# Kernel tuning notes

Measured on AMD Instinct MI355X. Metric: run time of the kernel, lower is better.

Reference implementation:

```python
import jax, jax.numpy as jnp
import numpy as np

DIM = 1024
SEQ_LEN = 2048
NUM_HEAD = 16
HEAD_DIM = 64
B = 4


def setup_inputs() -> dict:
    key = jax.random.key(0)
    ks = jax.random.split(key, 9)
    hd = NUM_HEAD * HEAD_DIM
    s_in = 1.0 / np.sqrt(DIM)
    s_o = 1.0 / np.sqrt(hd)
    return {
        "x": jax.random.normal(ks[0], (B, SEQ_LEN, DIM), dtype=jnp.float32),
        "q_w": jax.random.uniform(ks[1], (hd, DIM), jnp.float32, -s_in, s_in),
        "q_b": jax.random.uniform(ks[2], (hd,), jnp.float32, -s_in, s_in),
        "k_w": jax.random.uniform(ks[3], (hd, DIM), jnp.float32, -s_in, s_in),
        "k_b": jax.random.uniform(ks[4], (hd,), jnp.float32, -s_in, s_in),
        "v_w": jax.random.uniform(ks[5], (hd, DIM), jnp.float32, -s_in, s_in),
        "v_b": jax.random.uniform(ks[6], (hd,), jnp.float32, -s_in, s_in),
        "o_w": jax.random.uniform(ks[7], (DIM, hd), jnp.float32, -s_o, s_o),
        "o_b": jax.random.uniform(ks[8], (DIM,), jnp.float32, -s_o, s_o),
    }


def reference(x, q_w, q_b, k_w, k_b, v_w, v_b, o_w, o_b):
    Bn, T, C = x.shape
    # QKV projections (torch Linear: x @ W^T + b)
    q = (x @ q_w.T + q_b).reshape(Bn, T, NUM_HEAD, HEAD_DIM).transpose(0, 2, 1, 3)
    k = (x @ k_w.T + k_b).reshape(Bn, T, NUM_HEAD, HEAD_DIM).transpose(0, 2, 1, 3)
    v = (x @ v_w.T + v_b).reshape(Bn, T, NUM_HEAD, HEAD_DIM).transpose(0, 2, 1, 3)
    scale = HEAD_DIM ** -0.5
    attn = jnp.einsum("bhqd,bhkd->bhqk", q, k) * scale  # (B,H,T,T)
    causal = jnp.tril(jnp.ones((T, T), dtype=bool))
    attn = jnp.where(causal[None, None, :, :], attn, -jnp.inf)
    p = jax.nn.softmax(attn, axis=-1)  # stable softmax (max-subtracted)
    out = jnp.einsum("bhqk,bhkd->bhqd", p, v)
    out = out.transpose(0, 2, 1, 3).reshape(Bn, T, NUM_HEAD * HEAD_DIM)
    return out @ o_w.T + o_b
```

## Files before the change

### kernel.cpp

```cpp
#include <hip/hip_runtime.h>
#include <stdint.h>

typedef short short8 __attribute__((ext_vector_type(8)));
typedef float f32x4 __attribute__((ext_vector_type(4)));
typedef float f32x16 __attribute__((ext_vector_type(16)));
typedef unsigned int uint2v __attribute__((ext_vector_type(2)));
typedef unsigned int uint4v __attribute__((ext_vector_type(4)));

__device__ __forceinline__ unsigned short f2bf(float f) {
    unsigned int u = __float_as_uint(f);
    u += 0x7fffu + ((u >> 16) & 1u);
    return (unsigned short)(u >> 16);
}

__device__ __forceinline__ void gld_lds16(const unsigned short* g, unsigned short* l) {
    __builtin_amdgcn_global_load_lds((const __attribute__((address_space(1))) unsigned int*)g,
                                     (__attribute__((address_space(3))) unsigned int*)l,
                                     16, 0, 0);
}

#define QSCL 0.18033688011112042f

__global__ __launch_bounds__(256) void cvt_all(const float* __restrict__ x,
                                               const float* __restrict__ qw, const float* __restrict__ kw,
                                               const float* __restrict__ vw, const float* __restrict__ ow,
                                               const float* __restrict__ qb, const float* __restrict__ kb,
                                               const float* __restrict__ vb,
                                               unsigned short* __restrict__ Xb,
                                               unsigned short* __restrict__ Wqkv,
                                               unsigned short* __restrict__ Owb,
                                               float* __restrict__ bqkv) {
    int i = blockIdx.x * 256 + threadIdx.x;
    const float* src; uint2* dst; int j;
    if (i < 2097152)      { src = x;  dst = (uint2*)Xb;                j = i; }
    else if (i < 2359296) { src = qw; dst = (uint2*)Wqkv;              j = i - 2097152; }
    else if (i < 2621440) { src = kw; dst = (uint2*)(Wqkv + 1048576);  j = i - 2359296; }
    else if (i < 2883584) { src = vw; dst = (uint2*)(Wqkv + 2097152);  j = i - 2621440; }
    else if (i < 3145728) { src = ow; dst = (uint2*)Owb;               j = i - 2883584; }
    else {
        int t = i - 3145728;
        const float4* bs = (t < 256) ? (const float4*)qb : (t < 512) ? (const float4*)kb : (const float4*)vb;
        ((float4*)bqkv)[t] = bs[t & 255];
        return;
    }
    float4 v = ((const float4*)src)[j];
    unsigned int lo = (unsigned int)f2bf(v.x) | ((unsigned int)f2bf(v.y) << 16);
    unsigned int hi = (unsigned int)f2bf(v.z) | ((unsigned int)f2bf(v.w) << 16);
    dst[j] = make_uint2(lo, hi);
}

template<int MODE>
__global__ __launch_bounds__(256) void gemm_bt(const unsigned short* __restrict__ A,
                                               const unsigned short* __restrict__ Bm,
                                               const float* __restrict__ bias,
                                               void* __restrict__ C0,
                                               unsigned short* __restrict__ VtOut,
                                               int M, int N, int K)
{
    __shared__ __align__(16) unsigned short As[128 * 64];
    __shared__ __align__(16) unsigned short Bs[128 * 64];
    const int tid  = threadIdx.x;
    const int bm   = blockIdx.x, bn = blockIdx.y;
    const int lane = tid & 63, w = tid >> 6;
    const int wm   = w >> 1, wn = w & 1;
    const int quad = lane >> 4, l15 = lane & 15;

    f32x4 acc[4][4];
#pragma unroll
    for (int mt = 0; mt < 4; mt++)
#pragma unroll
        for (int nt = 0; nt < 4; nt++)
            acc[mt][nt] = (f32x4){0.f, 0.f, 0.f, 0.f};

    const int kTiles = K >> 6;
    for (int kt = 0; kt < kTiles; ++kt) {
        __syncthreads();
#pragma unroll
        for (int i = 0; i < 4; i++) {
            int G  = i * 256 + tid;
            int m  = G >> 3, g = G & 7;
            int gs = g ^ (m & 7);
            int Gb = i * 256 + (w << 6);
            gld_lds16(A  + (size_t)(bm * 128 + m) * K + kt * 64 + gs * 8, &As[Gb * 8]);
            gld_lds16(Bm + (size_t)(bn * 128 + m) * K + kt * 64 + gs * 8, &Bs[Gb * 8]);
        }
        __syncthreads();
#pragma unroll
        for (int ks = 0; ks < 2; ++ks) {
            short8 af[4], bfr[4];
#pragma unroll
            for (int mt = 0; mt < 4; mt++) {
                int m = wm * 64 + mt * 16 + l15;
                af[mt] = *(const short8*)&As[m * 64 + (((ks * 4 + quad) ^ (l15 & 7)) << 3)];
            }
#pragma unroll
            for (int nt = 0; nt < 4; nt++) {
                int n = wn * 64 + nt * 16 + l15;
                bfr[nt] = *(const short8*)&Bs[n * 64 + (((ks * 4 + quad) ^ (l15 & 7)) << 3)];
            }
#pragma unroll
            for (int mt = 0; mt < 4; mt++)
#pragma unroll
                for (int nt = 0; nt < 4; nt++)
                    acc[mt][nt] = __builtin_amdgcn_mfma_f32_16x16x32_bf16(af[mt], bfr[nt], acc[mt][nt], 0, 0, 0);
        }
    }
    const int row0 = bm * 128 + wm * 64, col0 = bn * 128 + wn * 64;
#pragma unroll
    for (int nt = 0; nt < 4; nt++) {
        int col = col0 + nt * 16 + l15;
        float bv = bias[col];
#pragma unroll
        for (int mt = 0; mt < 4; mt++) {
            if (MODE == 1 && col >= 2048) {
                int row = row0 + mt * 16 + quad * 4;
                int b = row >> 11, t = row & 2047;
                ushort4 pk;
                pk.x = f2bf(acc[mt][nt][0] + bv);
                pk.y = f2bf(acc[mt][nt][1] + bv);
                pk.z = f2bf(acc[mt][nt][2] + bv);
                pk.w = f2bf(acc[mt][nt][3] + bv);
                *(ushort4*)(VtOut + (size_t)(b * 1024 + (col - 2048)) * 2048 + t) = pk;
            } else {
#pragma unroll
                for (int r = 0; r < 4; r++) {
                    int row = row0 + mt * 16 + quad * 4 + r;
                    float v = acc[mt][nt][r] + bv;
                    if (MODE == 1) {
                        if (col < 1024) v *= QSCL;
                        ((unsigned short*)C0)[(size_t)row * 2048 + col] = f2bf(v);
                    } else {
                        ((float*)C0)[(size_t)row * N + col] = v;
                    }
                }
            }
        }
    }
}

#define NEG_RAW (-1e30f)
__global__ __launch_bounds__(256, 4) void attn_mfma(const unsigned short* __restrict__ QK,
                                                    const unsigned short* __restrict__ Vt,
                                                    unsigned short* __restrict__ O)
{
    __shared__ __align__(16) unsigned short Kb[3][64 * 64];
    __shared__ __align__(16) unsigned short Vb[3][64 * 64];
    const int tid  = threadIdx.x;
    const int lane = tid & 63, w = tid >> 6;
    const int hi   = lane >> 5, l31 = lane & 31;
    const int s7   = lane & 7;
    const int bh   = blockIdx.x;
    const int b    = bh >> 4, h = bh & 15;
    const int qt   = (int)gridDim.y - 1 - (int)blockIdx.y;
    const int qbase = qt * 128 + w * 32;

    const unsigned short* Qp = QK + (size_t)(b * 2048) * 2048 + h * 64;
    const unsigned short* Kp = Qp + 1024;
    const unsigned short* Vp = Vt + (size_t)(bh * 64) * 2048;

    short8 qf[4];
    {
        const unsigned short* qrow = Qp + (size_t)(qbase + l31) * 2048 + hi * 8;
#pragma unroll
        for (int dk = 0; dk < 4; dk++)
            qf[dk] = *(const short8*)(qrow + dk * 16);
    }

    f32x16 oacc[2];
#pragma unroll
    for (int i = 0; i < 2; i++)
#pragma unroll
        for (int r = 0; r < 16; r++) oacc[i][r] = 0.f;
    float lsum = 0.f;

    const int ktend   = 2 * qt + 1;
    const int ktmax_w = (qbase + 31) >> 6;

    auto stage = [&](int t, int bi) {
#pragma unroll
        for (int i = 0; i < 2; i++) {
            int G = i * 256 + tid;
            int r = G >> 3, g = G & 7, gs = g ^ (r & 7);
            int Gb = i * 256 + (w << 6);
            gld_lds16(Kp + (size_t)(t * 64 + r) * 2048 + gs * 8, &Kb[bi][Gb * 8]);
            gld_lds16(Vp + (size_t)r * 2048 + t * 64 + gs * 8, &Vb[bi][Gb * 8]);
        }
    };

    stage(0, 0);
    stage(1, 1);

    int cur = 0;
    for (int kt = 0; kt <= ktend; ++kt) {
        if (kt < ktend) asm volatile("s_waitcnt vmcnt(4)" ::: "memory");
        else            asm volatile("s_waitcnt vmcnt(0)" ::: "memory");
        __builtin_amdgcn_sched_barrier(0);
        __builtin_amdgcn_s_barrier();
        __builtin_amdgcn_sched_barrier(0);
        if (kt + 2 <= ktend) {
            int bi = cur + 2; if (bi >= 3) bi -= 3;
            stage(kt + 2, bi);
        }
        if (kt <= ktmax_w) {
            __builtin_amdgcn_s_setprio(1);
            const unsigned short* Kc = Kb[cur];
            const unsigned short* Vc = Vb[cur];
            const int kbase = kt * 64;
#pragma unroll
            for (int sub = 0; sub < 2; sub++) {
                const int kb0 = kbase + sub * 32;
                if (kb0 > qbase + 31) continue;
                f32x16 sacc;
#pragma unroll
                for (int r = 0; r < 16; r++) sacc[r] = 0.f;
                const unsigned short* kr = &Kc[(sub * 32 + l31) * 64];
#pragma unroll
                for (int dk = 0; dk < 4; dk++) {
                    short8 kf = *(const short8*)(kr + (((dk * 2 + hi) ^ s7) << 3));
                    sacc = __builtin_amdgcn_mfma_f32_32x32x16_bf16(kf, qf[dk], sacc, 0, 0, 0);
                }
                if (kb0 + 31 > qbase) {
                    const int qg = qbase + l31;
                    const int kb = kb0 + 4 * hi;
#pragma unroll
                    for (int r = 0; r < 16; r++) {
                        int key = kb + (r & 3) + 8 * (r >> 2);
                        if (key > qg) sacc[r] = NEG_RAW;
                    }
                }
#pragma unroll
                for (int r = 0; r < 16; r++) sacc[r] = __builtin_exp2f(sacc[r]);
                {
                    float s0 = (sacc[0] + sacc[1]) + (sacc[2] + sacc[3]);
                    float s1 = (sacc[4] + sacc[5]) + (sacc[6] + sacc[7]);
                    float s2 = (sacc[8] + sacc[9]) + (sacc[10] + sacc[11]);
                    float s3 = (sacc[12] + sacc[13]) + (sacc[14] + sacc[15]);
                    lsum += (s0 + s1) + (s2 + s3);
                }
                unsigned int pk[8];
#pragma unroll
                for (int t2 = 0; t2 < 8; t2++)
                    pk[t2] = __builtin_amdgcn_perm(__float_as_uint(sacc[2 * t2 + 1]),
                                                   __float_as_uint(sacc[2 * t2]), 0x07060302u);
                uint2v r0 = __builtin_amdgcn_permlane32_swap(pk[0], pk[2], false, false);
                uint2v r1 = __builtin_amdgcn_permlane32_swap(pk[1], pk[3], false, false);
                uint2v r2 = __builtin_amdgcn_permlane32_swap(pk[4], pk[6], false, false);
                uint2v r3 = __builtin_amdgcn_permlane32_swap(pk[5], pk[7], false, false);
                short8 pf[2];
                { uint4v u; u.x = r0.x; u.y = r1.x; u.z = r0.y; u.w = r1.y; pf[0] = __builtin_bit_cast(short8, u); }
                { uint4v u; u.x = r2.x; u.y = r3.x; u.z = r2.y; u.w = r3.y; pf[1] = __builtin_bit_cast(short8, u); }
#pragma unroll
                for (int kv = 0; kv < 2; kv++) {
#pragma unroll
                    for (int dsub = 0; dsub < 2; dsub++) {
                        const int d = dsub * 32 + l31;
                        short8 vf = *(const short8*)&Vc[d * 64 + (((sub * 4 + kv * 2 + hi) ^ s7) << 3)];
                        oacc[dsub] = __builtin_amdgcn_mfma_f32_32x32x16_bf16(vf, pf[kv], oacc[dsub], 0, 0, 0);
                    }
                }
            }
            __builtin_amdgcn_s_setprio(0);
        }
        cur = (cur == 2) ? 0 : cur + 1;
    }

    uint2v lt = __builtin_amdgcn_permlane32_swap(__float_as_uint(lsum), __float_as_uint(lsum), false, false);
    const float inv = 1.f / (__uint_as_float(lt.x) + __uint_as_float(lt.y));
    unsigned short* op = O + (size_t)(b * 2048 + qbase + l31) * 1024 + h * 64;
#pragma unroll
    for (int dsub = 0; dsub < 2; dsub++) {
#pragma unroll
        for (int q4 = 0; q4 < 4; q4++) {
            ushort4 pkv;
            pkv.x = f2bf(oacc[dsub][q4 * 4 + 0] * inv);
            pkv.y = f2bf(oacc[dsub][q4 * 4 + 1] * inv);
            pkv.z = f2bf(oacc[dsub][q4 * 4 + 2] * inv);
            pkv.w = f2bf(oacc[dsub][q4 * 4 + 3] * inv);
            *(ushort4*)(op + dsub * 32 + q4 * 8 + hi * 4) = pkv;
        }
    }
}

extern "C" void kernel_launch(void* const* d_in, const int* in_sizes, int n_in,
                              void* d_out, int out_size, void* d_ws, size_t ws_size,
                              hipStream_t stream)
{
    const float* x   = (const float*)d_in[0];
    const float* q_w = (const float*)d_in[1];
    const float* q_b = (const float*)d_in[2];
    const float* k_w = (const float*)d_in[3];
    const float* k_b = (const float*)d_in[4];
    const float* v_w = (const float*)d_in[5];
    const float* v_b = (const float*)d_in[6];
    const float* o_w = (const float*)d_in[7];
    const float* o_b = (const float*)d_in[8];
    float* out = (float*)d_out;

    unsigned short* Xb   = (unsigned short*)d_ws;
    unsigned short* Wqkv = Xb + 8388608;
    unsigned short* Owb  = Wqkv + 3145728;
    float*          bqkv = (float*)(Owb + 1048576);
    unsigned short* QK   = (unsigned short*)(bqkv + 3072);
    unsigned short* Vtg  = QK + 16777216;
    unsigned short* Abf  = Vtg + 8388608;

    cvt_all<<<12291, 256, 0, stream>>>(x, q_w, k_w, v_w, o_w, q_b, k_b, v_b,
                                       Xb, Wqkv, Owb, bqkv);
    gemm_bt<1><<<dim3(64, 24), 256, 0, stream>>>(Xb, Wqkv, bqkv, QK, Vtg, 8192, 3072, 1024);
    attn_mfma<<<dim3(64, 16), 256, 0, stream>>>(QK, Vtg, Abf);
    gemm_bt<0><<<dim3(64, 8), 256, 0, stream>>>(Abf, Owb, o_b, out, nullptr, 8192, 1024, 1024);
}
```

Before: 255.2 us.

## Replace QKV projection GEMM with 256x256-tile, 8-wave pipelined kernel

After: 265.4 us. 1.04x slower.

```diff
diff --git a/kernel.cpp b/kernel.cpp
--- a/kernel.cpp
+++ b/kernel.cpp
@@ -138,6 +138,154 @@
     }
 }
 
+#define PIN() __builtin_amdgcn_sched_barrier(0)
+
+#define RD_A(BI, MH) \
+    _Pragma("unroll") for (int mtl = 0; mtl < 4; ++mtl) { \
+        int m = wm * 128 + (MH) * 64 + mtl * 16 + l15; \
+        af[mtl][0] = *(const short8*)&As[BI][m * 64 + ((quad ^ (m & 7)) << 3)]; \
+        af[mtl][1] = *(const short8*)&As[BI][m * 64 + (((4 + quad) ^ (m & 7)) << 3)]; \
+    }
+
+#define RD_B(BI, NH) \
+    _Pragma("unroll") for (int ntl = 0; ntl < 2; ++ntl) { \
+        int n = wn * 64 + ((NH) * 2 + ntl) * 16 + l15; \
+        bfv[(NH) * 2 + ntl][0] = *(const short8*)&Bs[BI][n * 64 + ((quad ^ (n & 7)) << 3)]; \
+        bfv[(NH) * 2 + ntl][1] = *(const short8*)&Bs[BI][n * 64 + (((4 + quad) ^ (n & 7)) << 3)]; \
+    }
+
+#define MFMA_Q(MH, NH) \
+    __builtin_amdgcn_s_barrier(); \
+    asm volatile("s_waitcnt lgkmcnt(0)" ::: "memory"); \
+    PIN(); \
+    __builtin_amdgcn_s_setprio(1); \
+    _Pragma("unroll") for (int mtl = 0; mtl < 4; ++mtl) \
+    _Pragma("unroll") for (int ntl = 0; ntl < 2; ++ntl) { \
+        const int nt_ = (NH) * 2 + ntl, mt_ = (MH) * 4 + mtl; \
+        acc[mt_][nt_] = __builtin_amdgcn_mfma_f32_16x16x32_bf16(af[mtl][0], bfv[nt_][0], acc[mt_][nt_], 0, 0, 0); \
+        acc[mt_][nt_] = __builtin_amdgcn_mfma_f32_16x16x32_bf16(af[mtl][1], bfv[nt_][1], acc[mt_][nt_], 0, 0, 0); \
+    } \
+    __builtin_amdgcn_s_setprio(0);
+
+#define ENDP() do { __builtin_amdgcn_s_barrier(); PIN(); } while (0)
+
+#define STAGE(DST, BI, H, SRC, KT) \
+    _Pragma("unroll") for (int i_ = 0; i_ < 2; ++i_) { \
+        int G_ = i_ * 512 + tid; \
+        int r_ = G_ >> 3, g_ = G_ & 7, gs_ = g_ ^ (r_ & 7); \
+        gld_lds16((SRC) + (size_t)((H) * 128 + r_) * K + (KT) * 64 + gs_ * 8, \
+                  &DST[BI][(H) * 8192 + (i_ * 512 + w * 64) * 8]); \
+    }
+
+template<int MODE>
+__global__ __launch_bounds__(512, 2) void gemm256(const unsigned short* __restrict__ A,
+                                                  const unsigned short* __restrict__ Bm,
+                                                  const float* __restrict__ bias,
+                                                  void* __restrict__ C0,
+                                                  unsigned short* __restrict__ VtOut,
+                                                  int M, int N, int K)
+{
+    __shared__ __align__(16) unsigned short As[2][256 * 64];
+    __shared__ __align__(16) unsigned short Bs[2][256 * 64];
+    const int tid  = threadIdx.x;
+    const int bm   = blockIdx.x, bn = blockIdx.y;
+    const int lane = tid & 63, w = tid >> 6;
+    const int wm   = w >> 2, wn = w & 3;
+    const int quad = lane >> 4, l15 = lane & 15;
+
+    const unsigned short* Ag = A  + (size_t)(bm * 256) * K;
+    const unsigned short* Bg = Bm + (size_t)(bn * 256) * K;
+
+    f32x4 acc[8][4];
+#pragma unroll
+    for (int mt = 0; mt < 8; mt++)
+#pragma unroll
+        for (int nt = 0; nt < 4; nt++)
+            acc[mt][nt] = (f32x4){0.f, 0.f, 0.f, 0.f};
+
+    short8 af[4][2];
+    short8 bfv[4][2];
+
+    const int NI = K >> 7;
+
+    STAGE(As, 0, 0, Ag, 0); STAGE(As, 0, 1, Ag, 0);
+    STAGE(Bs, 0, 0, Bg, 0); STAGE(Bs, 0, 1, Bg, 0);
+    STAGE(Bs, 1, 0, Bg, 1); STAGE(Bs, 1, 1, Bg, 1);
+    STAGE(As, 1, 0, Ag, 1); STAGE(As, 1, 1, Ag, 1);
+    asm volatile("s_waitcnt vmcnt(8)" ::: "memory");
+    __builtin_amdgcn_s_barrier();
+    PIN();
+
+    for (int j = 0; j < NI; ++j) {
+        const int t2 = 2 * j + 2, t3 = 2 * j + 3;
+        const bool more = (j < NI - 1);
+        RD_A(0, 0); RD_B(0, 0);
+        MFMA_Q(0, 0);
+        ENDP();
+        RD_B(0, 1);
+        MFMA_Q(0, 1);
+        ENDP();
+        RD_A(0, 1);
+        if (more) { STAGE(Bs, 0, 0, Bg, t2); }
+        MFMA_Q(1, 0);
+        ENDP();
+        if (more) { STAGE(Bs, 0, 1, Bg, t2); }
+        MFMA_Q(1, 1);
+        if (more) { asm volatile("s_waitcnt vmcnt(4)" ::: "memory"); }
+        else      { asm volatile("s_waitcnt vmcnt(0)" ::: "memory"); }
+        ENDP();
+        RD_A(1, 0); RD_B(1, 0);
+        if (more) { STAGE(As, 0, 0, Ag, t2); }
+        MFMA_Q(0, 0);
+        ENDP();
+        RD_B(1, 1);
+        if (more) { STAGE(As, 0, 1, Ag, t2); }
+        MFMA_Q(0, 1);
+        ENDP();
+        RD_A(1, 1);
+        if (more) { STAGE(Bs, 1, 0, Bg, t3); STAGE(Bs, 1, 1, Bg, t3); }
+        MFMA_Q(1, 0);
+        ENDP();
+        if (more) { STAGE(As, 1, 0, Ag, t3); STAGE(As, 1, 1, Ag, t3); }
+        MFMA_Q(1, 1);
+        if (more) { asm volatile("s_waitcnt vmcnt(8)" ::: "memory"); }
+        else      { asm volatile("s_waitcnt vmcnt(0)" ::: "memory"); }
+        ENDP();
+    }
+
+    const int row0 = bm * 256 + wm * 128, col0 = bn * 256 + wn * 64;
+#pragma unroll
+    for (int nt = 0; nt < 4; nt++) {
+        int col = col0 + nt * 16 + l15;
+        float bv = bias[col];
+#pragma unroll
+        for (int mt = 0; mt < 8; mt++) {
+            if (MODE == 1 && col >= 2048) {
+                int row = row0 + mt * 16 + quad * 4;
+                int b = row >> 11, t = row & 2047;
+                ushort4 pk;
+                pk.x = f2bf(acc[mt][nt][0] + bv);
+                pk.y = f2bf(acc[mt][nt][1] + bv);
+                pk.z = f2bf(acc[mt][nt][2] + bv);
+                pk.w = f2bf(acc[mt][nt][3] + bv);
+                *(ushort4*)(VtOut + (size_t)(b * 1024 + (col - 2048)) * 2048 + t) = pk;
+            } else {
+#pragma unroll
+                for (int r = 0; r < 4; r++) {
+                    int row = row0 + mt * 16 + quad * 4 + r;
+                    float v = acc[mt][nt][r] + bv;
+                    if (MODE == 1) {
+                        if (col < 1024) v *= QSCL;
+                        ((unsigned short*)C0)[(size_t)row * 2048 + col] = f2bf(v);
+                    } else {
+                        ((float*)C0)[(size_t)row * N + col] = v;
+                    }
+                }
+            }
+        }
+    }
+}
+
 #define NEG_RAW (-1e30f)
 __global__ __launch_bounds__(256, 4) void attn_mfma(const unsigned short* __restrict__ QK,
                                                     const unsigned short* __restrict__ Vt,
@@ -306,7 +454,7 @@
 
     cvt_all<<<12291, 256, 0, stream>>>(x, q_w, k_w, v_w, o_w, q_b, k_b, v_b,
                                        Xb, Wqkv, Owb, bqkv);
-    gemm_bt<1><<<dim3(64, 24), 256, 0, stream>>>(Xb, Wqkv, bqkv, QK, Vtg, 8192, 3072, 1024);
+    gemm256<1><<<dim3(32, 12), 512, 0, stream>>>(Xb, Wqkv, bqkv, QK, Vtg, 8192, 3072, 1024);
     attn_mfma<<<dim3(64, 16), 256, 0, stream>>>(QK, Vtg, Abf);
     gemm_bt<0><<<dim3(64, 8), 256, 0, stream>>>(Abf, Owb, o_b, out, nullptr, 8192, 1024, 1024);
 }
```

## Double attention query tile per wave and pair causal tiles for load balance

Applied to the files above, without the earlier changes.

Result: slower. 272.8 us (+6.9%).

```diff
diff --git a/kernel.cpp b/kernel.cpp
--- a/kernel.cpp
+++ b/kernel.cpp
@@ -139,7 +139,7 @@
 }
 
 #define NEG_RAW (-1e30f)
-__global__ __launch_bounds__(256, 4) void attn_mfma(const unsigned short* __restrict__ QK,
+__global__ __launch_bounds__(256, 2) void attn_mfma(const unsigned short* __restrict__ QK,
                                                     const unsigned short* __restrict__ Vt,
                                                     unsigned short* __restrict__ O)
 {
@@ -149,38 +149,43 @@
     const int lane = tid & 63, w = tid >> 6;
     const int hi   = lane >> 5, l31 = lane & 31;
     const int s7   = lane & 7;
-    const int bh   = blockIdx.x;
+    const int bid  = (int)blockIdx.x;
+    const int bh   = bid & 63;
+    const int G    = bid >> 6;
+    const int qt   = (G < 4) ? (7 - G) : (G - 4);
     const int b    = bh >> 4, h = bh & 15;
-    const int qt   = (int)gridDim.y - 1 - (int)blockIdx.y;
-    const int qbase = qt * 128 + w * 32;
+    const int qbase = qt * 256 + w * 64;
 
     const unsigned short* Qp = QK + (size_t)(b * 2048) * 2048 + h * 64;
     const unsigned short* Kp = Qp + 1024;
     const unsigned short* Vp = Vt + (size_t)(bh * 64) * 2048;
 
-    short8 qf[4];
-    {
-        const unsigned short* qrow = Qp + (size_t)(qbase + l31) * 2048 + hi * 8;
+    short8 qf[2][4];
+#pragma unroll
+    for (int qsub = 0; qsub < 2; qsub++) {
+        const unsigned short* qrow = Qp + (size_t)(qbase + qsub * 32 + l31) * 2048 + hi * 8;
 #pragma unroll
         for (int dk = 0; dk < 4; dk++)
-            qf[dk] = *(const short8*)(qrow + dk * 16);
-    }
-
-    f32x16 oacc[2];
-#pragma unroll
-    for (int i = 0; i < 2; i++)
-#pragma unroll
-        for (int r = 0; r < 16; r++) oacc[i][r] = 0.f;
-    float lsum = 0.f;
-
-    const int ktend   = 2 * qt + 1;
-    const int ktmax_w = (qbase + 31) >> 6;
+            qf[qsub][dk] = *(const short8*)(qrow + dk * 16);
+    }
+
+    f32x16 oacc[2][2];
+#pragma unroll
+    for (int qsub = 0; qsub < 2; qsub++)
+#pragma unroll
+        for (int i = 0; i < 2; i++)
+#pragma unroll
+            for (int r = 0; r < 16; r++) oacc[qsub][i][r] = 0.f;
+    float lsum0 = 0.f, lsum1 = 0.f;
+
+    const int ktend   = 4 * qt + 3;
+    const int ktmax_w = (qbase + 63) >> 6;
 
     auto stage = [&](int t, int bi) {
 #pragma unroll
         for (int i = 0; i < 2; i++) {
-            int G = i * 256 + tid;
-            int r = G >> 3, g = G & 7, gs = g ^ (r & 7);
+            int G_ = i * 256 + tid;
+            int r = G_ >> 3, g = G_ & 7, gs = g ^ (r & 7);
             int Gb = i * 256 + (w << 6);
             gld_lds16(Kp + (size_t)(t * 64 + r) * 2048 + gs * 8, &Kb[bi][Gb * 8]);
             gld_lds16(Vp + (size_t)r * 2048 + t * 64 + gs * 8, &Vb[bi][Gb * 8]);
@@ -209,53 +214,66 @@
 #pragma unroll
             for (int sub = 0; sub < 2; sub++) {
                 const int kb0 = kbase + sub * 32;
-                if (kb0 > qbase + 31) continue;
-                f32x16 sacc;
-#pragma unroll
-                for (int r = 0; r < 16; r++) sacc[r] = 0.f;
-                const unsigned short* kr = &Kc[(sub * 32 + l31) * 64];
-#pragma unroll
-                for (int dk = 0; dk < 4; dk++) {
-                    short8 kf = *(const short8*)(kr + (((dk * 2 + hi) ^ s7) << 3));
-                    sacc = __builtin_amdgcn_mfma_f32_32x32x16_bf16(kf, qf[dk], sacc, 0, 0, 0);
+                if (kb0 > qbase + 63) continue;
+                short8 kf[4];
+                {
+                    const unsigned short* kr = &Kc[(sub * 32 + l31) * 64];
+#pragma unroll
+                    for (int dk = 0; dk < 4; dk++)
+                        kf[dk] = *(const short8*)(kr + (((dk * 2 + hi) ^ s7) << 3));
                 }
-                if (kb0 + 31 > qbase) {
-                    const int qg = qbase + l31;
-                    const int kb = kb0 + 4 * hi;
-#pragma unroll
-                    for (int r = 0; r < 16; r++) {
-                        int key = kb + (r & 3) + 8 * (r >> 2);
-                        if (key > qg) sacc[r] = NEG_RAW;
+                short8 pf[2][2];
+                bool contrib[2];
+#pragma unroll
+                for (int qsub = 0; qsub < 2; qsub++) {
+                    const int qb_s = qbase + qsub * 32;
+                    contrib[qsub] = (kb0 <= qb_s + 31);
+                    if (!contrib[qsub]) continue;
+                    f32x16 sacc;
+#pragma unroll
+                    for (int r = 0; r < 16; r++) sacc[r] = 0.f;
+#pragma unroll
+                    for (int dk = 0; dk < 4; dk++)
+                        sacc = __builtin_amdgcn_mfma_f32_32x32x16_bf16(kf[dk], qf[qsub][dk], sacc, 0, 0, 0);
+                    if (kb0 + 31 > qb_s) {
+                        const int qg = qb_s + l31;
+                        const int kb = kb0 + 4 * hi;
+#pragma unroll
+                        for (int r = 0; r < 16; r++) {
+                            int key = kb + (r & 3) + 8 * (r >> 2);
+                            if (key > qg) sacc[r] = NEG_RAW;
+                        }
                     }
+#pragma unroll
+                    for (int r = 0; r < 16; r++) sacc[r] = __builtin_exp2f(sacc[r]);
+                    {
+                        float s0 = (sacc[0] + sacc[1]) + (sacc[2] + sacc[3]);
+                        float s1 = (sacc[4] + sacc[5]) + (sacc[6] + sacc[7]);
+                        float s2 = (sacc[8] + sacc[9]) + (sacc[10] + sacc[11]);
+                        float s3 = (sacc[12] + sacc[13]) + (sacc[14] + sacc[15]);
+                        if (qsub == 0) lsum0 += (s0 + s1) + (s2 + s3);
+                        else           lsum1 += (s0 + s1) + (s2 + s3);
+                    }
+                    unsigned int pk[8];
+#pragma unroll
+                    for (int t2 = 0; t2 < 8; t2++)
+                        pk[t2] = __builtin_amdgcn_perm(__float_as_uint(sacc[2 * t2 + 1]),
+                                                       __float_as_uint(sacc[2 * t2]), 0x07060302u);
+                    uint2v r0 = __builtin_amdgcn_permlane32_swap(pk[0], pk[2], false, false);
+                    uint2v r1 = __builtin_amdgcn_permlane32_swap(pk[1], pk[3], false, false);
+                    uint2v r2 = __builtin_amdgcn_permlane32_swap(pk[4], pk[6], false, false);
+                    uint2v r3 = __builtin_amdgcn_permlane32_swap(pk[5], pk[7], false, false);
+                    { uint4v u; u.x = r0.x; u.y = r1.x; u.z = r0.y; u.w = r1.y; pf[qsub][0] = __builtin_bit_cast(short8, u); }
+                    { uint4v u; u.x = r2.x; u.y = r3.x; u.z = r2.y; u.w = r3.y; pf[qsub][1] = __builtin_bit_cast(short8, u); }
                 }
-#pragma unroll
-                for (int r = 0; r < 16; r++) sacc[r] = __builtin_exp2f(sacc[r]);
-                {
-                    float s0 = (sacc[0] + sacc[1]) + (sacc[2] + sacc[3]);
-                    float s1 = (sacc[4] + sacc[5]) + (sacc[6] + sacc[7]);
-                    float s2 = (sacc[8] + sacc[9]) + (sacc[10] + sacc[11]);
-                    float s3 = (sacc[12] + sacc[13]) + (sacc[14] + sacc[15]);
-                    lsum += (s0 + s1) + (s2 + s3);
-                }
-                unsigned int pk[8];
-#pragma unroll
-                for (int t2 = 0; t2 < 8; t2++)
-                    pk[t2] = __builtin_amdgcn_perm(__float_as_uint(sacc[2 * t2 + 1]),
-                                                   __float_as_uint(sacc[2 * t2]), 0x07060302u);
-                uint2v r0 = __builtin_amdgcn_permlane32_swap(pk[0], pk[2], false, false);
-                uint2v r1 = __builtin_amdgcn_permlane32_swap(pk[1], pk[3], false, false);
-                uint2v r2 = __builtin_amdgcn_permlane32_swap(pk[4], pk[6], false, false);
-                uint2v r3 = __builtin_amdgcn_permlane32_swap(pk[5], pk[7], false, false);
-                short8 pf[2];
-                { uint4v u; u.x = r0.x; u.y = r1.x; u.z = r0.y; u.w = r1.y; pf[0] = __builtin_bit_cast(short8, u); }
-                { uint4v u; u.x = r2.x; u.y = r3.x; u.z = r2.y; u.w = r3.y; pf[1] = __builtin_bit_cast(short8, u); }
 #pragma unroll
                 for (int kv = 0; kv < 2; kv++) {
 #pragma unroll
                     for (int dsub = 0; dsub < 2; dsub++) {
                         const int d = dsub * 32 + l31;
                         short8 vf = *(const short8*)&Vc[d * 64 + (((sub * 4 + kv * 2 + hi) ^ s7) << 3)];
-                        oacc[dsub] = __builtin_amdgcn_mfma_f32_32x32x16_bf16(vf, pf[kv], oacc[dsub], 0, 0, 0);
+                        if (contrib[0]) oacc[0][dsub] = __builtin_amdgcn_mfma_f32_32x32x16_bf16(vf, pf[0][kv], oacc[0][dsub], 0, 0, 0);
+                        if (contrib[1]) oacc[1][dsub] = __builtin_amdgcn_mfma_f32_32x32x16_bf16(vf, pf[1][kv], oacc[1][dsub], 0, 0, 0);
                     }
                 }
             }
@@ -264,19 +282,23 @@
         cur = (cur == 2) ? 0 : cur + 1;
     }
 
-    uint2v lt = __builtin_amdgcn_permlane32_swap(__float_as_uint(lsum), __float_as_uint(lsum), false, false);
-    const float inv = 1.f / (__uint_as_float(lt.x) + __uint_as_float(lt.y));
-    unsigned short* op = O + (size_t)(b * 2048 + qbase + l31) * 1024 + h * 64;
-#pragma unroll
-    for (int dsub = 0; dsub < 2; dsub++) {
-#pragma unroll
-        for (int q4 = 0; q4 < 4; q4++) {
-            ushort4 pkv;
-            pkv.x = f2bf(oacc[dsub][q4 * 4 + 0] * inv);
-            pkv.y = f2bf(oacc[dsub][q4 * 4 + 1] * inv);
-            pkv.z = f2bf(oacc[dsub][q4 * 4 + 2] * inv);
-            pkv.w = f2bf(oacc[dsub][q4 * 4 + 3] * inv);
-            *(ushort4*)(op + dsub * 32 + q4 * 8 + hi * 4) = pkv;
+#pragma unroll
+    for (int qsub = 0; qsub < 2; qsub++) {
+        float ls = qsub ? lsum1 : lsum0;
+        uint2v lt = __builtin_amdgcn_permlane32_swap(__float_as_uint(ls), __float_as_uint(ls), false, false);
+        const float inv = 1.f / (__uint_as_float(lt.x) + __uint_as_float(lt.y));
+        unsigned short* op = O + (size_t)(b * 2048 + qbase + qsub * 32 + l31) * 1024 + h * 64;
+#pragma unroll
+        for (int dsub = 0; dsub < 2; dsub++) {
+#pragma unroll
+            for (int q4 = 0; q4 < 4; q4++) {
+                ushort4 pkv;
+                pkv.x = f2bf(oacc[qsub][dsub][q4 * 4 + 0] * inv);
+                pkv.y = f2bf(oacc[qsub][dsub][q4 * 4 + 1] * inv);
+                pkv.z = f2bf(oacc[qsub][dsub][q4 * 4 + 2] * inv);
+                pkv.w = f2bf(oacc[qsub][dsub][q4 * 4 + 3] * inv);
+                *(ushort4*)(op + dsub * 32 + q4 * 8 + hi * 4) = pkv;
+            }
         }
     }
 }
@@ -307,6 +329,6 @@
     cvt_all<<<12291, 256, 0, stream>>>(x, q_w, k_w, v_w, o_w, q_b, k_b, v_b,
                                        Xb, Wqkv, Owb, bqkv);
     gemm_bt<1><<<dim3(64, 24), 256, 0, stream>>>(Xb, Wqkv, bqkv, QK, Vtg, 8192, 3072, 1024);
-    attn_mfma<<<dim3(64, 16), 256, 0, stream>>>(QK, Vtg, Abf);
+    attn_mfma<<<512, 256, 0, stream>>>(QK, Vtg, Abf);
     gemm_bt<0><<<dim3(64, 8), 256, 0, stream>>>(Abf, Owb, o_b, out, nullptr, 8192, 1024, 1024);
 }
```

## Use 32x32 MFMA in projection GEMM and compute softmax row sums via MFMA

Applied to the files above, without the earlier changes.

Result: no change. 256.0 us (+0.3%).

```diff
diff --git a/kernel.cpp b/kernel.cpp
--- a/kernel.cpp
+++ b/kernel.cpp
@@ -63,14 +63,16 @@
     const int bm   = blockIdx.x, bn = blockIdx.y;
     const int lane = tid & 63, w = tid >> 6;
     const int wm   = w >> 1, wn = w & 1;
-    const int quad = lane >> 4, l15 = lane & 15;
-
-    f32x4 acc[4][4];
-#pragma unroll
-    for (int mt = 0; mt < 4; mt++)
-#pragma unroll
-        for (int nt = 0; nt < 4; nt++)
-            acc[mt][nt] = (f32x4){0.f, 0.f, 0.f, 0.f};
+    const int hi   = lane >> 5, l31 = lane & 31;
+
+    f32x16 acc[2][2];
+#pragma unroll
+    for (int mt = 0; mt < 2; mt++)
+#pragma unroll
+        for (int nt = 0; nt < 2; nt++)
+#pragma unroll
+            for (int r = 0; r < 16; r++)
+                acc[mt][nt][r] = 0.f;
 
     const int kTiles = K >> 6;
     for (int kt = 0; kt < kTiles; ++kt) {
@@ -86,45 +88,48 @@
         }
         __syncthreads();
 #pragma unroll
-        for (int ks = 0; ks < 2; ++ks) {
-            short8 af[4], bfr[4];
-#pragma unroll
-            for (int mt = 0; mt < 4; mt++) {
-                int m = wm * 64 + mt * 16 + l15;
-                af[mt] = *(const short8*)&As[m * 64 + (((ks * 4 + quad) ^ (l15 & 7)) << 3)];
+        for (int ks = 0; ks < 4; ++ks) {
+            short8 af[2], bfr[2];
+#pragma unroll
+            for (int mt = 0; mt < 2; mt++) {
+                int m = wm * 64 + mt * 32 + l31;
+                af[mt] = *(const short8*)&As[m * 64 + (((ks * 2 + hi) ^ (m & 7)) << 3)];
             }
 #pragma unroll
-            for (int nt = 0; nt < 4; nt++) {
-                int n = wn * 64 + nt * 16 + l15;
-                bfr[nt] = *(const short8*)&Bs[n * 64 + (((ks * 4 + quad) ^ (l15 & 7)) << 3)];
+            for (int nt = 0; nt < 2; nt++) {
+                int n = wn * 64 + nt * 32 + l31;
+                bfr[nt] = *(const short8*)&Bs[n * 64 + (((ks * 2 + hi) ^ (n & 7)) << 3)];
             }
 #pragma unroll
-            for (int mt = 0; mt < 4; mt++)
-#pragma unroll
-                for (int nt = 0; nt < 4; nt++)
-                    acc[mt][nt] = __builtin_amdgcn_mfma_f32_16x16x32_bf16(af[mt], bfr[nt], acc[mt][nt], 0, 0, 0);
+            for (int mt = 0; mt < 2; mt++)
+#pragma unroll
+                for (int nt = 0; nt < 2; nt++)
+                    acc[mt][nt] = __builtin_amdgcn_mfma_f32_32x32x16_bf16(af[mt], bfr[nt], acc[mt][nt], 0, 0, 0);
         }
     }
     const int row0 = bm * 128 + wm * 64, col0 = bn * 128 + wn * 64;
 #pragma unroll
-    for (int nt = 0; nt < 4; nt++) {
-        int col = col0 + nt * 16 + l15;
+    for (int nt = 0; nt < 2; nt++) {
+        int col = col0 + nt * 32 + l31;
         float bv = bias[col];
 #pragma unroll
-        for (int mt = 0; mt < 4; mt++) {
+        for (int mt = 0; mt < 2; mt++) {
             if (MODE == 1 && col >= 2048) {
-                int row = row0 + mt * 16 + quad * 4;
-                int b = row >> 11, t = row & 2047;
-                ushort4 pk;
-                pk.x = f2bf(acc[mt][nt][0] + bv);
-                pk.y = f2bf(acc[mt][nt][1] + bv);
-                pk.z = f2bf(acc[mt][nt][2] + bv);
-                pk.w = f2bf(acc[mt][nt][3] + bv);
-                *(ushort4*)(VtOut + (size_t)(b * 1024 + (col - 2048)) * 2048 + t) = pk;
+#pragma unroll
+                for (int r4 = 0; r4 < 4; r4++) {
+                    int row = row0 + mt * 32 + r4 * 8 + hi * 4;
+                    int b = row >> 11, t = row & 2047;
+                    ushort4 pk;
+                    pk.x = f2bf(acc[mt][nt][r4 * 4 + 0] + bv);
+                    pk.y = f2bf(acc[mt][nt][r4 * 4 + 1] + bv);
+                    pk.z = f2bf(acc[mt][nt][r4 * 4 + 2] + bv);
+                    pk.w = f2bf(acc[mt][nt][r4 * 4 + 3] + bv);
+                    *(ushort4*)(VtOut + (size_t)(b * 1024 + (col - 2048)) * 2048 + t) = pk;
+                }
             } else {
 #pragma unroll
-                for (int r = 0; r < 4; r++) {
-                    int row = row0 + mt * 16 + quad * 4 + r;
+                for (int r = 0; r < 16; r++) {
+                    int row = row0 + mt * 32 + (r & 3) + 8 * (r >> 2) + 4 * hi;
                     float v = acc[mt][nt][r] + bv;
                     if (MODE == 1) {
                         if (col < 1024) v *= QSCL;
@@ -166,12 +171,17 @@
             qf[dk] = *(const short8*)(qrow + dk * 16);
     }
 
-    f32x16 oacc[2];
+    short8 ones;
+#pragma unroll
+    for (int j = 0; j < 8; j++) ones[j] = (short)0x3F80;
+
+    f32x16 oacc[2], lacc;
 #pragma unroll
     for (int i = 0; i < 2; i++)
 #pragma unroll
         for (int r = 0; r < 16; r++) oacc[i][r] = 0.f;
-    float lsum = 0.f;
+#pragma unroll
+    for (int r = 0; r < 16; r++) lacc[r] = 0.f;
 
     const int ktend   = 2 * qt + 1;
     const int ktmax_w = (qbase + 31) >> 6;
@@ -230,13 +240,6 @@
                 }
 #pragma unroll
                 for (int r = 0; r < 16; r++) sacc[r] = __builtin_exp2f(sacc[r]);
-                {
-                    float s0 = (sacc[0] + sacc[1]) + (sacc[2] + sacc[3]);
-                    float s1 = (sacc[4] + sacc[5]) + (sacc[6] + sacc[7]);
-                    float s2 = (sacc[8] + sacc[9]) + (sacc[10] + sacc[11]);
-                    float s3 = (sacc[12] + sacc[13]) + (sacc[14] + sacc[15]);
-                    lsum += (s0 + s1) + (s2 + s3);
-                }
                 unsigned int pk[8];
 #pragma unroll
                 for (int t2 = 0; t2 < 8; t2++)
@@ -251,6 +254,7 @@
                 { uint4v u; u.x = r2.x; u.y = r3.x; u.z = r2.y; u.w = r3.y; pf[1] = __builtin_bit_cast(short8, u); }
 #pragma unroll
                 for (int kv = 0; kv < 2; kv++) {
+                    lacc = __builtin_amdgcn_mfma_f32_32x32x16_bf16(ones, pf[kv], lacc, 0, 0, 0);
 #pragma unroll
                     for (int dsub = 0; dsub < 2; dsub++) {
                         const int d = dsub * 32 + l31;
@@ -264,8 +268,7 @@
         cur = (cur == 2) ? 0 : cur + 1;
     }
 
-    uint2v lt = __builtin_amdgcn_permlane32_swap(__float_as_uint(lsum), __float_as_uint(lsum), false, false);
-    const float inv = 1.f / (__uint_as_float(lt.x) + __uint_as_float(lt.y));
+    const float inv = 1.f / lacc[0];
     unsigned short* op = O + (size_t)(b * 2048 + qbase + l31) * 1024 + h * 64;
 #pragma unroll
     for (int dsub = 0; dsub < 2; dsub++) {
```
